# Optimization experiments

Measured on AMD Instinct MI355X. Metric: run time of the kernel, lower is better.

## Reference

```python
import jax, jax.numpy as jnp
import numpy as np

E = 200_000        # num edges (messages)
T = 2_000_000      # num triplets
H = 128            # hidden_channels
I = 64             # int_emb_size
B = 8              # basis_emb_size
NR = 6             # num_radial
NS = 7             # num_spherical
NB_BEFORE = 1
NB_AFTER = 2


def _glorot(key, shape, scale=2.0):
    fan = shape[0] + shape[1]
    std = jnp.sqrt(scale * 2.0 / fan)
    return jax.random.normal(key, shape, dtype=jnp.float32) * std


def setup_inputs() -> dict:
    key = jax.random.key(0)
    ks = jax.random.split(key, 20)
    inp = {
        "x": jax.random.normal(ks[0], (E, H), dtype=jnp.float32),
        "rbf": jax.random.uniform(ks[1], (E, NR), dtype=jnp.float32),
        "sbf": jax.random.uniform(ks[2], (T, NS * NR), dtype=jnp.float32),
        "idx_kj": jax.random.randint(ks[3], (T,), 0, E),
        "idx_ji": jax.random.randint(ks[4], (T,), 0, E),
        # weights stored as [in, out] so forward is x @ W
        "W_rbf1": _glorot(ks[5], (NR, B)),
        "W_rbf2": _glorot(ks[6], (B, H)),
        "W_sbf1": _glorot(ks[7], (NS * NR, B)),
        "W_sbf2": _glorot(ks[8], (B, I)),
        "W_kj": _glorot(ks[9], (H, H)),
        "b_kj": jnp.zeros((H,), dtype=jnp.float32),
        "W_ji": _glorot(ks[10], (H, H)),
        "b_ji": jnp.zeros((H,), dtype=jnp.float32),
        "W_down": _glorot(ks[11], (H, I)),
        "W_up": _glorot(ks[12], (I, H)),
        # residual layers: [n_layers, 2, H, H] weights, [n_layers, 2, H] biases
        "W_res_before": jnp.stack([jnp.stack([_glorot(jax.random.fold_in(ks[13], 2 * l + m), (H, H)) for m in range(2)]) for l in range(NB_BEFORE)]),
        "b_res_before": jnp.zeros((NB_BEFORE, 2, H), dtype=jnp.float32),
        "W_lin": _glorot(ks[14], (H, H)),
        "b_lin": jnp.zeros((H,), dtype=jnp.float32),
        "W_res_after": jnp.stack([jnp.stack([_glorot(jax.random.fold_in(ks[15], 2 * l + m), (H, H)) for m in range(2)]) for l in range(NB_AFTER)]),
        "b_res_after": jnp.zeros((NB_AFTER, 2, H), dtype=jnp.float32),
    }
    return inp


def _residual_stack(h, Ws, bs):
    # h: [E,H]; Ws: [L,2,H,H]; bs: [L,2,H]
    for l in range(Ws.shape[0]):
        inner = jax.nn.silu(h @ Ws[l, 0] + bs[l, 0])
        h = h + jax.nn.silu(inner @ Ws[l, 1] + bs[l, 1])
    return h


def reference(x, rbf, sbf, idx_kj, idx_ji,
              W_rbf1, W_rbf2, W_sbf1, W_sbf2,
              W_kj, b_kj, W_ji, b_ji, W_down, W_up,
              W_res_before, b_res_before, W_lin, b_lin,
              W_res_after, b_res_after):
    act = jax.nn.silu  # swish
    x_ji = act(x @ W_ji + b_ji)                    # [E,H]
    x_kj = act(x @ W_kj + b_kj)                    # [E,H]
    rbf_e = (rbf @ W_rbf1) @ W_rbf2                # [E,H]
    x_kj = x_kj * rbf_e
    x_kj = act(x_kj @ W_down)                      # [E,I]
    sbf_e = (sbf @ W_sbf1) @ W_sbf2                # [T,I]
    m = x_kj[idx_kj] * sbf_e                       # [T,I] gather + basis weight
    agg = jax.ops.segment_sum(m, idx_ji, num_segments=x.shape[0])  # [E,I] scatter-add
    x_kj = act(agg @ W_up)                         # [E,H]
    h = x_ji + x_kj
    h = _residual_stack(h, W_res_before, b_res_before)
    h = act(h @ W_lin + b_lin) + x                 # skip connection
    h = _residual_stack(h, W_res_after, b_res_after)
    return h
```

## Files before the change

### kernel.cpp

```cpp
#include <hip/hip_runtime.h>
#include <math.h>
#include <stdint.h>

#define SCHUNK 2048
#define PCH 128

typedef __bf16 bf16x8 __attribute__((ext_vector_type(8)));
typedef __bf16 bf16x4 __attribute__((ext_vector_type(4)));
typedef float f32x4 __attribute__((ext_vector_type(4)));

#define MFMA16(a, b, c) __builtin_amdgcn_mfma_f32_16x16x32_bf16(a, b, c, 0, 0, 0)

#define OFF_KJ    0
#define OFF_JI    16384
#define OFF_DOWN  32768
#define OFF_UP    40960
#define OFF_RB0   49152
#define OFF_RB1   65536
#define OFF_LIN   81920
#define OFF_RA00  98304
#define OFF_RA01  114688
#define OFF_RA10  131072
#define OFF_RA11  147456

__device__ __forceinline__ float silu_f(float v) {
    return v * __builtin_amdgcn_rcpf(1.0f + __expf(-v));
}

template<int K, int NB, int STRIDE, int NTOT>
__device__ __forceinline__ void wgemm(const __bf16* __restrict__ At,
                                      const __bf16* __restrict__ Wf,
                                      int ct0, int lane, f32x4* __restrict__ acc) {
#pragma unroll
    for (int i = 0; i < NB; ++i) acc[i] = (f32x4){0.f, 0.f, 0.f, 0.f};
    const int rl = lane & 15;
    const int kq = (lane >> 4) * 8;
    const int sw = (rl & 7) << 3;
#pragma unroll
    for (int kc = 0; kc < K / 32; ++kc) {
        const int k0 = kc * 32 + kq;
        bf16x8 b = *(const bf16x8*)&Wf[(size_t)((kc * NTOT + ct0) * 64 + lane) * 8];
#pragma unroll
        for (int s = 0; s < NB; ++s) {
            bf16x8 a = *(const bf16x8*)&At[(rl + 16 * s) * STRIDE + (k0 ^ sw)];
            acc[s] = MFMA16(a, b, acc[s]);
        }
    }
}

template<int COLS, int NTHR>
__device__ __forceinline__ void stage(const float* __restrict__ g, long grow0,
                                      int vr, __bf16* __restrict__ At, int tid) {
    constexpr int QUADS = COLS / 4;
#pragma unroll
    for (int i = tid; i < 64 * QUADS; i += NTHR) {
        int r = i / QUADS, q = i - r * QUADS;
        float4 v = make_float4(0.f, 0.f, 0.f, 0.f);
        if (r < vr) v = *(const float4*)&g[(grow0 + r) * (size_t)COLS + q * 4];
        bf16x4 w; w[0] = (__bf16)v.x; w[1] = (__bf16)v.y; w[2] = (__bf16)v.z; w[3] = (__bf16)v.w;
        *(bf16x4*)&At[r * 128 + ((q * 4) ^ ((r & 7) << 3))] = w;
    }
}

template<int COLS, int NTHR>
__device__ __forceinline__ void stage_bf(const __bf16* __restrict__ g, long grow0,
                                         int vr, __bf16* __restrict__ At, int tid) {
    constexpr int CH = COLS / 8;
#pragma unroll
    for (int i = tid; i < 64 * CH; i += NTHR) {
        int r = i / CH, q = i - r * CH;
        bf16x8 v = (bf16x8){0, 0, 0, 0, 0, 0, 0, 0};
        if (r < vr) v = *(const bf16x8*)&g[(grow0 + r) * (size_t)COLS + q * 8];
        *(bf16x8*)&At[r * 128 + ((q * 8) ^ ((r & 7) << 3))] = v;
    }
}

__device__ __forceinline__ void epi_store(__bf16* __restrict__ At, const f32x4* __restrict__ acc,
                                          const float* __restrict__ bias, int lane, int colbase) {
    const int rl = lane & 15, rg = (lane >> 4) << 2;
    const int col = colbase + rl;
    const float bv = bias[col];
#pragma unroll
    for (int s = 0; s < 4; ++s)
#pragma unroll
        for (int j = 0; j < 4; ++j) {
            const int row = s * 16 + rg + j;
            At[row * 128 + (col ^ ((row & 7) << 3))] = (__bf16)silu_f(acc[s][j] + bv);
        }
}

template<bool WRITE>
__device__ __forceinline__ void epi_add(__bf16* __restrict__ At, f32x4* __restrict__ hreg,
                                        const f32x4* __restrict__ acc,
                                        const float* __restrict__ bias, int lane, int colbase) {
    const int rl = lane & 15, rg = (lane >> 4) << 2;
    const int col = colbase + rl;
    const float bv = bias[col];
#pragma unroll
    for (int s = 0; s < 4; ++s)
#pragma unroll
        for (int j = 0; j < 4; ++j) {
            const int row = s * 16 + rg + j;
            float v = hreg[s][j] + silu_f(acc[s][j] + bv);
            hreg[s][j] = v;
            if (WRITE) At[row * 128 + (col ^ ((row & 7) << 3))] = (__bf16)v;
        }
}

__global__ void kweights(const float* __restrict__ W_rbf1, const float* __restrict__ W_rbf2,
                         const float* __restrict__ W_sbf1, const float* __restrict__ W_sbf2,
                         float* __restrict__ wcrT, float* __restrict__ wc_sbf,
                         __bf16* __restrict__ wcsb) {
    int tid = blockIdx.x * blockDim.x + threadIdx.x;
    int nt = blockDim.x * gridDim.x;
    for (int idx = tid; idx < 128 * 8; idx += nt) {
        int c = idx >> 3, s = idx & 7;
        float v = 0.f;
        if (s < 6) {
#pragma unroll
            for (int b = 0; b < 8; ++b) v += W_rbf1[s * 8 + b] * W_rbf2[b * 128 + c];
        }
        wcrT[idx] = v;
    }
    for (int idx = tid; idx < 42 * 64; idx += nt) {
        int r = idx / 64, c = idx - r * 64;
        float s = 0.f;
#pragma unroll
        for (int b = 0; b < 8; ++b) s += W_sbf1[r * 8 + b] * W_sbf2[b * 64 + c];
        wc_sbf[idx] = s;
    }
    for (int idx = tid; idx < 4096; idx += nt) {
        int j = idx & 7, l = (idx >> 3) & 63, r2 = idx >> 9;
        int ct = r2 & 3, kc = r2 >> 2;
        int k = kc * 32 + ((l >> 4) << 3) + j;
        int c = ct * 16 + (l & 15);
        float v = 0.f;
        if (k < 42) {
#pragma unroll
            for (int b = 0; b < 8; ++b) v += W_sbf1[k * 8 + b] * W_sbf2[b * 64 + c];
        }
        wcsb[idx] = (__bf16)v;
    }
}

__global__ void ktrans(const float* __restrict__ W_kj, const float* __restrict__ W_ji,
                       const float* __restrict__ W_down, const float* __restrict__ W_up,
                       const float* __restrict__ W_rb, const float* __restrict__ W_lin,
                       const float* __restrict__ W_ra, __bf16* __restrict__ wt) {
    const float* src; __bf16* dst; int K, N;
    switch (blockIdx.y) {
        case 0:  src = W_kj;          dst = wt + OFF_KJ;    K = 128; N = 128; break;
        case 1:  src = W_ji;          dst = wt + OFF_JI;    K = 128; N = 128; break;
        case 2:  src = W_down;        dst = wt + OFF_DOWN;  K = 128; N = 64;  break;
        case 3:  src = W_up;          dst = wt + OFF_UP;    K = 64;  N = 128; break;
        case 4:  src = W_rb;          dst = wt + OFF_RB0;   K = 128; N = 128; break;
        case 5:  src = W_rb + 16384;  dst = wt + OFF_RB1;   K = 128; N = 128; break;
        case 6:  src = W_lin;         dst = wt + OFF_LIN;   K = 128; N = 128; break;
        case 7:  src = W_ra;          dst = wt + OFF_RA00;  K = 128; N = 128; break;
        case 8:  src = W_ra + 16384;  dst = wt + OFF_RA01;  K = 128; N = 128; break;
        case 9:  src = W_ra + 32768;  dst = wt + OFF_RA10;  K = 128; N = 128; break;
        default: src = W_ra + 49152;  dst = wt + OFF_RA11;  K = 128; N = 128; break;
    }
    const int ntot = N / 16;
    for (int i = blockIdx.x * blockDim.x + threadIdx.x; i < K * N; i += gridDim.x * blockDim.x) {
        int j = i & 7, l = (i >> 3) & 63, r2 = i >> 9;
        int ct = r2 % ntot, kc = r2 / ntot;
        int k = kc * 32 + ((l >> 4) << 3) + j;
        int n = ct * 16 + (l & 15);
        dst[i] = (__bf16)src[(size_t)k * N + n];
    }
}

__global__ __launch_bounds__(512, 4) void kpre_m(
        const float* __restrict__ x, const float* __restrict__ rbf,
        const __bf16* __restrict__ wt, const float* __restrict__ b_kj,
        const float* __restrict__ wcrT, __bf16* __restrict__ xkd, int E) {
    __shared__ __bf16 A0[64 * 128];
    __shared__ __bf16 A1[64 * 128];
    __shared__ float rbt[64 * 8];
    const int tid = threadIdx.x, lane = tid & 63, wv = tid >> 6;
    const long r0 = (long)blockIdx.x * 64;
    if (r0 >= E) return;
    const int vr = (E - r0) < 64 ? (int)(E - r0) : 64;
    const int rl = lane & 15, rg = (lane >> 4) << 2;
    const int col = wv * 16 + rl;

    stage<128, 512>(x, r0, vr, A0, tid);
    for (int i = tid; i < 64 * 8; i += 512) {
        int r = i >> 3, s = i & 7;
        rbt[i] = (s < 6 && r < vr) ? rbf[(r0 + r) * 6 + s] : 0.f;
    }
    __syncthreads();

    f32x4 acc[4];
    wgemm<128, 4, 128, 8>(A0, wt + OFF_KJ, wv, lane, acc);

    const float bv = b_kj[col];
    float wv6[6];
#pragma unroll
    for (int s = 0; s < 6; ++s) wv6[s] = wcrT[col * 8 + s];
#pragma unroll
    for (int s = 0; s < 4; ++s)
#pragma unroll
        for (int j = 0; j < 4; ++j) {
            const int row = s * 16 + rg + j;
            float4 r4 = *(const float4*)&rbt[row * 8];
            float2 r2 = *(const float2*)&rbt[row * 8 + 4];
            float re = r4.x * wv6[0] + r4.y * wv6[1] + r4.z * wv6[2]
                     + r4.w * wv6[3] + r2.x * wv6[4] + r2.y * wv6[5];
            float v = silu_f(acc[s][j] + bv) * re;
            A1[row * 128 + (col ^ ((row & 7) << 3))] = (__bf16)v;
        }
    __syncthreads();

    const int hw = wv >> 2, ct = wv & 3;
    f32x4 acc2[2];
    wgemm<128, 2, 128, 4>(A1 + hw * 32 * 128, wt + OFF_DOWN, ct, lane, acc2);
    const int col2 = ct * 16 + rl;
#pragma unroll
    for (int s = 0; s < 2; ++s)
#pragma unroll
        for (int j = 0; j < 4; ++j) {
            const int row = hw * 32 + s * 16 + rg + j;
            if (row < vr) xkd[(r0 + row) * 64 + col2] = (__bf16)silu_f(acc2[s][j]);
        }
}

__global__ __launch_bounds__(512, 4) void kpost_m(
        const float* __restrict__ x, const __bf16* __restrict__ agg,
        const __bf16* __restrict__ mperm, const int* __restrict__ rs,
        const __bf16* __restrict__ wt, const float* __restrict__ b_ji,
        const float* __restrict__ b_rb, const float* __restrict__ b_lin,
        const float* __restrict__ b_ra, float* __restrict__ out, int E,
        int use_mperm) {
    __shared__ __bf16 A0[64 * 128];
    __shared__ __bf16 A1[64 * 128];
    const int tid = threadIdx.x, lane = tid & 63, wv = tid >> 6;
    const int colbase = wv * 16;
    const long r0 = (long)blockIdx.x * 64;
    if (r0 >= E) return;
    const int vr = (E - r0) < 64 ? (int)(E - r0) : 64;
    const int rl = lane & 15, rg = (lane >> 4) << 2;
    const int col = colbase + rl;
    f32x4 acc[4], hreg[4];

    stage<128, 512>(x, r0, vr, A1, tid);

    if (use_mperm) {
        const int el = tid >> 3, oct = tid & 7;
        const long e = r0 + el;
        float s0[8], s1[8];
#pragma unroll
        for (int k = 0; k < 8; ++k) { s0[k] = 0.f; s1[k] = 0.f; }
        if (el < vr) {
            const int j0 = rs[e], j1 = rs[e + 1];
            const __bf16* pm = mperm + (size_t)j0 * 64 + oct * 8;
            const int n = j1 - j0;
            int j = 0;
            for (; j + 2 <= n; j += 2) {
                bf16x8 v0 = *(const bf16x8*)&pm[(size_t)j * 64];
                bf16x8 v1 = *(const bf16x8*)&pm[(size_t)(j + 1) * 64];
#pragma unroll
                for (int k = 0; k < 8; ++k) { s0[k] += (float)v0[k]; s1[k] += (float)v1[k]; }
            }
            if (j < n) {
                bf16x8 v0 = *(const bf16x8*)&pm[(size_t)j * 64];
#pragma unroll
                for (int k = 0; k < 8; ++k) s0[k] += (float)v0[k];
            }
        }
        bf16x8 w;
#pragma unroll
        for (int k = 0; k < 8; ++k) w[k] = (__bf16)(s0[k] + s1[k]);
        *(bf16x8*)&A0[el * 128 + ((oct * 8) ^ ((el & 7) << 3))] = w;
    } else {
        stage_bf<64, 512>(agg, r0, vr, A0, tid);
    }
    __syncthreads();

    wgemm<64, 4, 128, 8>(A0, wt + OFF_UP, wv, lane, acc);
#pragma unroll
    for (int i = 0; i < 4; ++i)
#pragma unroll
        for (int j = 0; j < 4; ++j) hreg[i][j] = silu_f(acc[i][j]);
    wgemm<128, 4, 128, 8>(A1, wt + OFF_JI, wv, lane, acc);
    __syncthreads();
    epi_add<true>(A0, hreg, acc, b_ji, lane, colbase);
    __syncthreads();

    wgemm<128, 4, 128, 8>(A0, wt + OFF_RB0, wv, lane, acc);
    epi_store(A1, acc, b_rb, lane, colbase);
    __syncthreads();
    wgemm<128, 4, 128, 8>(A1, wt + OFF_RB1, wv, lane, acc);
    epi_add<true>(A0, hreg, acc, b_rb + 128, lane, colbase);
    __syncthreads();

    wgemm<128, 4, 128, 8>(A0, wt + OFF_LIN, wv, lane, acc);
    {
        const float bv = b_lin[col];
#pragma unroll
        for (int s = 0; s < 4; ++s)
#pragma unroll
            for (int j = 0; j < 4; ++j) {
                const int row = s * 16 + rg + j;
                float xv = (row < vr) ? x[(r0 + row) * 128 + col] : 0.f;
                float v = silu_f(acc[s][j] + bv) + xv;
                hreg[s][j] = v;
                A1[row * 128 + (col ^ ((row & 7) << 3))] = (__bf16)v;
            }
    }
    __syncthreads();

    wgemm<128, 4, 128, 8>(A1, wt + OFF_RA00, wv, lane, acc);
    epi_store(A0, acc, b_ra, lane, colbase);
    __syncthreads();
    wgemm<128, 4, 128, 8>(A0, wt + OFF_RA01, wv, lane, acc);
    epi_add<true>(A1, hreg, acc, b_ra + 128, lane, colbase);
    __syncthreads();

    wgemm<128, 4, 128, 8>(A1, wt + OFF_RA10, wv, lane, acc);
    epi_store(A0, acc, b_ra + 256, lane, colbase);
    __syncthreads();
    wgemm<128, 4, 128, 8>(A0, wt + OFF_RA11, wv, lane, acc);
    epi_add<false>(nullptr, hreg, acc, b_ra + 384, lane, colbase);

#pragma unroll
    for (int s = 0; s < 4; ++s)
#pragma unroll
        for (int j = 0; j < 4; ++j) {
            const int row = s * 16 + rg + j;
            if (row < vr) out[(r0 + row) * 128 + col] = hreg[s][j];
        }
}

__global__ void khist(const int* __restrict__ idx_ji, int* __restrict__ cnt, int T) {
    int t = blockIdx.x * blockDim.x + threadIdx.x;
    int nt = gridDim.x * blockDim.x;
    for (; t < T; t += nt) atomicAdd(&cnt[idx_ji[t]], 1);
}

__global__ __launch_bounds__(256) void kscan1(int* __restrict__ a, int* __restrict__ bsum) {
    __shared__ int sc[256];
    const int tid = threadIdx.x;
    const int base = blockIdx.x * SCHUNK + tid * 8;
    int4 p0 = *(const int4*)&a[base];
    int4 p1 = *(const int4*)&a[base + 4];
    int v[8] = {p0.x, p0.y, p0.z, p0.w, p1.x, p1.y, p1.z, p1.w};
    int s = 0;
#pragma unroll
    for (int i = 0; i < 8; ++i) s += v[i];
    sc[tid] = s;
    __syncthreads();
    for (int off = 1; off < 256; off <<= 1) {
        int t2 = (tid >= off) ? sc[tid - off] : 0;
        __syncthreads();
        sc[tid] += t2;
        __syncthreads();
    }
    int run = sc[tid] - s;
    if (tid == 255) bsum[blockIdx.x] = sc[255];
    int o[8];
#pragma unroll
    for (int i = 0; i < 8; ++i) { o[i] = run; run += v[i]; }
    *(int4*)&a[base]     = make_int4(o[0], o[1], o[2], o[3]);
    *(int4*)&a[base + 4] = make_int4(o[4], o[5], o[6], o[7]);
}

__global__ void kscan2(int* __restrict__ bsum, int nb) {
    if (threadIdx.x == 0 && blockIdx.x == 0) {
        int run = 0;
        for (int i = 0; i < nb; ++i) { int v = bsum[i]; bsum[i] = run; run += v; }
    }
}

__global__ void kscan3(int* __restrict__ a, const int* __restrict__ bsum,
                       int* __restrict__ cursor, int n) {
    int i = blockIdx.x * blockDim.x + threadIdx.x;
    if (i < n) {
        int v = a[i] + bsum[i >> 11];
        a[i] = v;
        cursor[i] = v;
    }
}

__global__ void kscatter(const int* __restrict__ idx_ji, int* __restrict__ cursor,
                         int* __restrict__ pos, int T) {
    int t = blockIdx.x * blockDim.x + threadIdx.x;
    int nt = gridDim.x * blockDim.x;
    for (; t < T; t += nt) {
        pos[t] = atomicAdd(&cursor[idx_ji[t]], 1);
    }
}

__global__ __launch_bounds__(512, 4) void kperm(
        const float* __restrict__ sbf, const int* __restrict__ idx_kj,
        const int* __restrict__ pos, const __bf16* __restrict__ xkd,
        const __bf16* __restrict__ wcsb, __bf16* __restrict__ mperm, int T) {
    __shared__ __bf16 S[PCH * 64];
    __shared__ __bf16 O[PCH * 72];
    __shared__ int kidx[PCH];
    __shared__ int posv[PCH];
    const int tid = threadIdx.x, lane = tid & 63, wv = tid >> 6;
    const long p0 = (long)blockIdx.x * PCH;
    const int np = (T - p0) > PCH ? PCH : (int)(T - p0);

    for (int i = tid; i < PCH * 64 / 8; i += 512)
        *(bf16x8*)&S[i * 8] = (bf16x8){0, 0, 0, 0, 0, 0, 0, 0};
    for (int i = tid; i < PCH; i += 512) {
        kidx[i] = (i < np) ? idx_kj[p0 + i] : 0;
        posv[i] = (i < np) ? pos[p0 + i] : 0;
    }
    __syncthreads();
    for (int i = tid; i < np * 21; i += 512) {
        int posi = i / 21, q = i - posi * 21;
        float2 v = *(const float2*)&sbf[(p0 + posi) * 42 + 2 * q];
        __bf16* d = &S[posi * 64 + ((2 * q) ^ ((posi & 7) << 3))];
        d[0] = (__bf16)v.x; d[1] = (__bf16)v.y;
    }
    __syncthreads();

    const int rh = wv & 1, ct = wv >> 1;
    f32x4 acc[4];
    wgemm<64, 4, 64, 4>(S + rh * 64 * 64, wcsb, ct, lane, acc);

    const int rl = lane & 15, rg = (lane >> 4) << 2;
    const int col = ct * 16 + rl;
#pragma unroll
    for (int s = 0; s < 4; ++s)
#pragma unroll
        for (int j = 0; j < 4; ++j) {
            const int r = rh * 64 + s * 16 + rg + j;
            const int kj = kidx[r];
            float xv = (float)xkd[(size_t)kj * 64 + col];
            O[r * 72 + col] = (__bf16)(acc[s][j] * xv);
        }
    __syncthreads();

    for (int i = tid; i < np * 8; i += 512) {
        int r = i >> 3, q = i & 7;
        size_t dst = (size_t)posv[r];
        *(bf16x8*)&mperm[dst * 64 + q * 8] = *(const bf16x8*)&O[r * 72 + q * 8];
    }
}

__global__ __launch_bounds__(256) void ktrip(
        const float* __restrict__ sbf, const int* __restrict__ idx_kj,
        const int* __restrict__ idx_ji, const __bf16* __restrict__ xkd,
        const float* __restrict__ wc_sbf, float* __restrict__ aggf, int T) {
    const int lane = threadIdx.x & 63;
    float wc[42];
#pragma unroll
    for (int s = 0; s < 42; ++s) wc[s] = wc_sbf[s * 64 + lane];
    const int wave = blockIdx.x * (blockDim.x >> 6) + (threadIdx.x >> 6);
    const int nw = gridDim.x * (blockDim.x >> 6);
    for (int t = wave; t < T; t += nw) {
        const float* srow = sbf + (size_t)t * 42;
        float acc = 0.f;
#pragma unroll
        for (int q = 0; q < 21; ++q) {
            float2 v = *(const float2*)&srow[q * 2];
            acc = fmaf(v.x, wc[q * 2 + 0], acc);
            acc = fmaf(v.y, wc[q * 2 + 1], acc);
        }
        int kj = idx_kj[t];
        int ji = idx_ji[t];
        float m = (float)xkd[(size_t)kj * 64 + lane] * acc;
        atomicAdd(&aggf[(size_t)ji * 64 + lane], m);
    }
}

__global__ void kcvt(const float* __restrict__ src, __bf16* __restrict__ dst, int n) {
    int i = blockIdx.x * blockDim.x + threadIdx.x;
    int nt = gridDim.x * blockDim.x;
    for (; i < n; i += nt) dst[i] = (__bf16)src[i];
}

static inline char* alignup256(char* p) {
    return (char*)(((uintptr_t)p + 255) & ~(uintptr_t)255);
}

extern "C" void kernel_launch(void* const* d_in, const int* in_sizes, int n_in,
                              void* d_out, int out_size, void* d_ws, size_t ws_size,
                              hipStream_t stream) {
    const float* x      = (const float*)d_in[0];
    const float* rbf    = (const float*)d_in[1];
    const float* sbf    = (const float*)d_in[2];
    const int*   idx_kj = (const int*)d_in[3];
    const int*   idx_ji = (const int*)d_in[4];
    const float* W_rbf1 = (const float*)d_in[5];
    const float* W_rbf2 = (const float*)d_in[6];
    const float* W_sbf1 = (const float*)d_in[7];
    const float* W_sbf2 = (const float*)d_in[8];
    const float* W_kj   = (const float*)d_in[9];
    const float* b_kj   = (const float*)d_in[10];
    const float* W_ji   = (const float*)d_in[11];
    const float* b_ji   = (const float*)d_in[12];
    const float* W_down = (const float*)d_in[13];
    const float* W_up   = (const float*)d_in[14];
    const float* W_rb   = (const float*)d_in[15];
    const float* b_rb   = (const float*)d_in[16];
    const float* W_lin  = (const float*)d_in[17];
    const float* b_lin  = (const float*)d_in[18];
    const float* W_ra   = (const float*)d_in[19];
    const float* b_ra   = (const float*)d_in[20];

    const int E = in_sizes[0] / 128;
    const int T = in_sizes[3];
    const int NB = (E + 1 + SCHUNK - 1) / SCHUNK;
    const int Epad = NB * SCHUNK;

    char* p = (char*)d_ws;
    __bf16* agg  = (__bf16*)p;  p = alignup256(p + (size_t)E * 64 * 2);
    __bf16* xkd  = (__bf16*)p;  p = alignup256(p + (size_t)E * 64 * 2);
    float* wcrT  = (float*)p;   p = alignup256(p + 1024 * 4);
    float* wcs   = (float*)p;   p = alignup256(p + 2688 * 4);
    __bf16* wcsb = (__bf16*)p;  p = alignup256(p + 4096 * 2);
    __bf16* wt   = (__bf16*)p;  p = alignup256(p + (size_t)163840 * 2);
    int* rs      = (int*)p;     p = alignup256(p + (size_t)Epad * 4);
    int* cursor  = (int*)p;     p = alignup256(p + (size_t)Epad * 4);
    int* bsum    = (int*)p;     p = alignup256(p + (size_t)NB * 4);
    int* pos     = (int*)p;     p = alignup256(p + (size_t)T * 4);
    __bf16* mperm = (__bf16*)p; p = alignup256(p + (size_t)T * 64 * 2);
    const bool fits = (size_t)(p - (char*)d_ws) <= ws_size;
    float* aggf = (float*)mperm;
    const bool fits_fb = (size_t)((char*)(aggf + (size_t)E * 64) - (char*)d_ws) <= ws_size;

    kweights<<<16, 256, 0, stream>>>(W_rbf1, W_rbf2, W_sbf1, W_sbf2, wcrT, wcs, wcsb);
    ktrans<<<dim3(16, 11), 256, 0, stream>>>(W_kj, W_ji, W_down, W_up, W_rb, W_lin, W_ra, wt);

    const int gE = (E + 63) / 64;
    kpre_m<<<gE, 512, 0, stream>>>(x, rbf, wt, b_kj, wcrT, xkd, E);

    if (fits) {
        hipMemsetAsync(rs, 0, (size_t)Epad * sizeof(int), stream);
        khist<<<2048, 256, 0, stream>>>(idx_ji, rs, T);
        kscan1<<<NB, 256, 0, stream>>>(rs, bsum);
        kscan2<<<1, 64, 0, stream>>>(bsum, NB);
        kscan3<<<(Epad + 255) / 256, 256, 0, stream>>>(rs, bsum, cursor, Epad);
        kscatter<<<2048, 256, 0, stream>>>(idx_ji, cursor, pos, T);
        kperm<<<(T + PCH - 1) / PCH, 512, 0, stream>>>(sbf, idx_kj, pos, xkd, wcsb, mperm, T);
        kpost_m<<<gE, 512, 0, stream>>>(x, agg, mperm, rs, wt, b_ji, b_rb, b_lin, b_ra,
                                        (float*)d_out, E, 1);
    } else if (fits_fb) {
        hipMemsetAsync(aggf, 0, (size_t)E * 64 * sizeof(float), stream);
        ktrip<<<2048, 256, 0, stream>>>(sbf, idx_kj, idx_ji, xkd, wcs, aggf, T);
        kcvt<<<2048, 256, 0, stream>>>(aggf, agg, E * 64);
        kpost_m<<<gE, 512, 0, stream>>>(x, agg, mperm, rs, wt, b_ji, b_rb, b_lin, b_ra,
                                        (float*)d_out, E, 0);
    }
}
```

Measured before the change: 594.5 us.

## Swap MFMA operands so accumulators hold row-contiguous columns for vector stores

```diff
diff --git a/kernel.cpp b/kernel.cpp
--- a/kernel.cpp
+++ b/kernel.cpp
@@ -39,11 +39,11 @@
 #pragma unroll
     for (int kc = 0; kc < K / 32; ++kc) {
         const int k0 = kc * 32 + kq;
-        bf16x8 b = *(const bf16x8*)&Wf[(size_t)((kc * NTOT + ct0) * 64 + lane) * 8];
+        bf16x8 wf = *(const bf16x8*)&Wf[(size_t)((kc * NTOT + ct0) * 64 + lane) * 8];
 #pragma unroll
         for (int s = 0; s < NB; ++s) {
-            bf16x8 a = *(const bf16x8*)&At[(rl + 16 * s) * STRIDE + (k0 ^ sw)];
-            acc[s] = MFMA16(a, b, acc[s]);
+            bf16x8 ef = *(const bf16x8*)&At[(rl + 16 * s) * STRIDE + (k0 ^ sw)];
+            acc[s] = MFMA16(wf, ef, acc[s]);
         }
     }
 }
@@ -78,15 +78,18 @@
 __device__ __forceinline__ void epi_store(__bf16* __restrict__ At, const f32x4* __restrict__ acc,
                                           const float* __restrict__ bias, int lane, int colbase) {
     const int rl = lane & 15, rg = (lane >> 4) << 2;
-    const int col = colbase + rl;
-    const float bv = bias[col];
-#pragma unroll
-    for (int s = 0; s < 4; ++s)
-#pragma unroll
-        for (int j = 0; j < 4; ++j) {
-            const int row = s * 16 + rg + j;
-            At[row * 128 + (col ^ ((row & 7) << 3))] = (__bf16)silu_f(acc[s][j] + bv);
-        }
+    const int cb = colbase + rg;
+    const float4 bv = *(const float4*)&bias[cb];
+#pragma unroll
+    for (int s = 0; s < 4; ++s) {
+        const int el = s * 16 + rl;
+        bf16x4 w;
+        w[0] = (__bf16)silu_f(acc[s][0] + bv.x);
+        w[1] = (__bf16)silu_f(acc[s][1] + bv.y);
+        w[2] = (__bf16)silu_f(acc[s][2] + bv.z);
+        w[3] = (__bf16)silu_f(acc[s][3] + bv.w);
+        *(bf16x4*)&At[el * 128 + (cb ^ ((el & 7) << 3))] = w;
+    }
 }
 
 template<bool WRITE>
@@ -94,17 +97,21 @@
                                         const f32x4* __restrict__ acc,
                                         const float* __restrict__ bias, int lane, int colbase) {
     const int rl = lane & 15, rg = (lane >> 4) << 2;
-    const int col = colbase + rl;
-    const float bv = bias[col];
-#pragma unroll
-    for (int s = 0; s < 4; ++s)
-#pragma unroll
-        for (int j = 0; j < 4; ++j) {
-            const int row = s * 16 + rg + j;
-            float v = hreg[s][j] + silu_f(acc[s][j] + bv);
-            hreg[s][j] = v;
-            if (WRITE) At[row * 128 + (col ^ ((row & 7) << 3))] = (__bf16)v;
-        }
+    const int cb = colbase + rg;
+    const float4 bv = *(const float4*)&bias[cb];
+#pragma unroll
+    for (int s = 0; s < 4; ++s) {
+        const int el = s * 16 + rl;
+        float v0 = hreg[s][0] + silu_f(acc[s][0] + bv.x);
+        float v1 = hreg[s][1] + silu_f(acc[s][1] + bv.y);
+        float v2 = hreg[s][2] + silu_f(acc[s][2] + bv.z);
+        float v3 = hreg[s][3] + silu_f(acc[s][3] + bv.w);
+        hreg[s][0] = v0; hreg[s][1] = v1; hreg[s][2] = v2; hreg[s][3] = v3;
+        if (WRITE) {
+            bf16x4 w; w[0] = (__bf16)v0; w[1] = (__bf16)v1; w[2] = (__bf16)v2; w[3] = (__bf16)v3;
+            *(bf16x4*)&At[el * 128 + (cb ^ ((el & 7) << 3))] = w;
+        }
+    }
 }
 
 __global__ void kweights(const float* __restrict__ W_rbf1, const float* __restrict__ W_rbf2,
@@ -179,11 +186,12 @@
     __shared__ __bf16 A1[64 * 128];
     __shared__ float rbt[64 * 8];
     const int tid = threadIdx.x, lane = tid & 63, wv = tid >> 6;
+    const int colbase = wv * 16;
     const long r0 = (long)blockIdx.x * 64;
     if (r0 >= E) return;
     const int vr = (E - r0) < 64 ? (int)(E - r0) : 64;
     const int rl = lane & 15, rg = (lane >> 4) << 2;
-    const int col = wv * 16 + rl;
+    const int cb = colbase + rg;
 
     stage<128, 512>(x, r0, vr, A0, tid);
     for (int i = tid; i < 64 * 8; i += 512) {
@@ -195,35 +203,46 @@
     f32x4 acc[4];
     wgemm<128, 4, 128, 8>(A0, wt + OFF_KJ, wv, lane, acc);
 
-    const float bv = b_kj[col];
-    float wv6[6];
-#pragma unroll
-    for (int s = 0; s < 6; ++s) wv6[s] = wcrT[col * 8 + s];
-#pragma unroll
-    for (int s = 0; s < 4; ++s)
+    const float4 bv = *(const float4*)&b_kj[cb];
+    float wcr[4][6];
+#pragma unroll
+    for (int j = 0; j < 4; ++j) {
+        float4 a4 = *(const float4*)&wcrT[(cb + j) * 8];
+        float2 a2 = *(const float2*)&wcrT[(cb + j) * 8 + 4];
+        wcr[j][0] = a4.x; wcr[j][1] = a4.y; wcr[j][2] = a4.z;
+        wcr[j][3] = a4.w; wcr[j][4] = a2.x; wcr[j][5] = a2.y;
+    }
+#pragma unroll
+    for (int s = 0; s < 4; ++s) {
+        const int el = s * 16 + rl;
+        float4 r4 = *(const float4*)&rbt[el * 8];
+        float2 r2 = *(const float2*)&rbt[el * 8 + 4];
+        float bb[4] = {bv.x, bv.y, bv.z, bv.w};
+        bf16x4 w;
 #pragma unroll
         for (int j = 0; j < 4; ++j) {
-            const int row = s * 16 + rg + j;
-            float4 r4 = *(const float4*)&rbt[row * 8];
-            float2 r2 = *(const float2*)&rbt[row * 8 + 4];
-            float re = r4.x * wv6[0] + r4.y * wv6[1] + r4.z * wv6[2]
-                     + r4.w * wv6[3] + r2.x * wv6[4] + r2.y * wv6[5];
-            float v = silu_f(acc[s][j] + bv) * re;
-            A1[row * 128 + (col ^ ((row & 7) << 3))] = (__bf16)v;
-        }
+            float re = r4.x * wcr[j][0] + r4.y * wcr[j][1] + r4.z * wcr[j][2]
+                     + r4.w * wcr[j][3] + r2.x * wcr[j][4] + r2.y * wcr[j][5];
+            w[j] = (__bf16)(silu_f(acc[s][j] + bb[j]) * re);
+        }
+        *(bf16x4*)&A1[el * 128 + (cb ^ ((el & 7) << 3))] = w;
+    }
     __syncthreads();
 
     const int hw = wv >> 2, ct = wv & 3;
+    const int cb2 = ct * 16 + rg;
     f32x4 acc2[2];
     wgemm<128, 2, 128, 4>(A1 + hw * 32 * 128, wt + OFF_DOWN, ct, lane, acc2);
-    const int col2 = ct * 16 + rl;
-#pragma unroll
-    for (int s = 0; s < 2; ++s)
-#pragma unroll
-        for (int j = 0; j < 4; ++j) {
-            const int row = hw * 32 + s * 16 + rg + j;
-            if (row < vr) xkd[(r0 + row) * 64 + col2] = (__bf16)silu_f(acc2[s][j]);
-        }
+#pragma unroll
+    for (int s = 0; s < 2; ++s) {
+        const int el = hw * 32 + s * 16 + rl;
+        if (el < vr) {
+            bf16x4 w;
+#pragma unroll
+            for (int j = 0; j < 4; ++j) w[j] = (__bf16)silu_f(acc2[s][j]);
+            *(bf16x4*)&xkd[(r0 + el) * 64 + cb2] = w;
+        }
+    }
 }
 
 __global__ __launch_bounds__(512, 4) void kpost_m(
@@ -241,7 +260,7 @@
     if (r0 >= E) return;
     const int vr = (E - r0) < 64 ? (int)(E - r0) : 64;
     const int rl = lane & 15, rg = (lane >> 4) << 2;
-    const int col = colbase + rl;
+    const int cb = colbase + rg;
     f32x4 acc[4], hreg[4];
 
     stage<128, 512>(x, r0, vr, A1, tid);
@@ -297,17 +316,23 @@
 
     wgemm<128, 4, 128, 8>(A0, wt + OFF_LIN, wv, lane, acc);
     {
-        const float bv = b_lin[col];
-#pragma unroll
-        for (int s = 0; s < 4; ++s)
+        const float4 bv = *(const float4*)&b_lin[cb];
+        const float bb[4] = {bv.x, bv.y, bv.z, bv.w};
+#pragma unroll
+        for (int s = 0; s < 4; ++s) {
+            const int el = s * 16 + rl;
+            float4 xv = make_float4(0.f, 0.f, 0.f, 0.f);
+            if (el < vr) xv = *(const float4*)&x[(r0 + el) * 128 + cb];
+            const float xx[4] = {xv.x, xv.y, xv.z, xv.w};
+            bf16x4 w;
 #pragma unroll
             for (int j = 0; j < 4; ++j) {
-                const int row = s * 16 + rg + j;
-                float xv = (row < vr) ? x[(r0 + row) * 128 + col] : 0.f;
-                float v = silu_f(acc[s][j] + bv) + xv;
+                float v = silu_f(acc[s][j] + bb[j]) + xx[j];
                 hreg[s][j] = v;
-                A1[row * 128 + (col ^ ((row & 7) << 3))] = (__bf16)v;
+                w[j] = (__bf16)v;
             }
+            *(bf16x4*)&A1[el * 128 + (cb ^ ((el & 7) << 3))] = w;
+        }
     }
     __syncthreads();
 
@@ -325,12 +350,10 @@
     epi_add<false>(nullptr, hreg, acc, b_ra + 384, lane, colbase);
 
 #pragma unroll
-    for (int s = 0; s < 4; ++s)
-#pragma unroll
-        for (int j = 0; j < 4; ++j) {
-            const int row = s * 16 + rg + j;
-            if (row < vr) out[(r0 + row) * 128 + col] = hreg[s][j];
-        }
+    for (int s = 0; s < 4; ++s) {
+        const int el = s * 16 + rl;
+        if (el < vr) *(f32x4*)&out[(r0 + el) * 128 + cb] = hreg[s];
+    }
 }
 
 __global__ void khist(const int* __restrict__ idx_ji, int* __restrict__ cnt, int T) {
@@ -424,16 +447,17 @@
     wgemm<64, 4, 64, 4>(S + rh * 64 * 64, wcsb, ct, lane, acc);
 
     const int rl = lane & 15, rg = (lane >> 4) << 2;
-    const int col = ct * 16 + rl;
-#pragma unroll
-    for (int s = 0; s < 4; ++s)
-#pragma unroll
-        for (int j = 0; j < 4; ++j) {
-            const int r = rh * 64 + s * 16 + rg + j;
-            const int kj = kidx[r];
-            float xv = (float)xkd[(size_t)kj * 64 + col];
-            O[r * 72 + col] = (__bf16)(acc[s][j] * xv);
-        }
+    const int cb = ct * 16 + rg;
+#pragma unroll
+    for (int s = 0; s < 4; ++s) {
+        const int r = rh * 64 + s * 16 + rl;
+        const int kj = kidx[r];
+        bf16x4 xk = *(const bf16x4*)&xkd[(size_t)kj * 64 + cb];
+        bf16x4 w;
+#pragma unroll
+        for (int j = 0; j < 4; ++j) w[j] = (__bf16)(acc[s][j] * (float)xk[j]);
+        *(bf16x4*)&O[r * 72 + cb] = w;
+    }
     __syncthreads();
 
     for (int i = tid; i < np * 8; i += 512) {
```

After: 569.2 us. -4.3%, faster.
